# Optimization experiments

Hardware: AMD Instinct MI355X
Metric: run time of the kernel (lower is better)

Reference implementation:

```python
import jax, jax.numpy as jnp
import numpy as np

D_MODEL = 512
NUM_HEADS = 8


def setup_inputs() -> dict:
    key = jax.random.key(0)
    ks = jax.random.split(key, 6)
    B, S, D = 4, 2048, D_MODEL
    Q = jax.random.normal(ks[0], (B, S, D), dtype=jnp.float32)
    K = jax.random.normal(ks[1], (B, S, D), dtype=jnp.float32)
    V = jax.random.normal(ks[2], (B, S, D), dtype=jnp.float32)
    # boolean mask, True = masked out; random so no row is fully masked
    mask = jax.random.randint(ks[3], (B, S, S), 0, 2).astype(jnp.bool_)
    scale = 1.0 / np.sqrt(D)
    Wq = jax.random.normal(ks[4], (D, D), dtype=jnp.float32) * scale
    Wo = jax.random.normal(ks[5], (D, D), dtype=jnp.float32) * scale
    return {"Q": Q, "K": K, "V": V, "mask": mask, "Wq": Wq, "Wo": Wo}


def reference(Q, K, V, mask, Wq, Wo):
    B, S, D = Q.shape
    H = NUM_HEADS
    dk = D // H
    # Faithful to the source: Q_Linear's weight (Wq) is applied to Q, K AND V
    # (K_Linear / V_Linear are dead parameters in the original module).
    q = (Q @ Wq.T).reshape(B, S, H, dk)
    k = (K @ Wq.T).reshape(B, S, H, dk)
    v = (V @ Wq.T).reshape(B, S, H, dk)
    # scores: [B, H, Sq, Sk]
    scores = jnp.einsum("bqhd,bkhd->bhqk", q, k)
    scores = jnp.where(mask[:, None, :, :], -jnp.inf, scores)
    w = jax.nn.softmax(scores / jnp.sqrt(jnp.asarray(dk, scores.dtype)), axis=-1)
    c = jnp.einsum("bhqk,bkhd->bqhd", w, v).reshape(B, S, D)
    return c @ Wo.T
```

## Files before the change

kernel.cpp:

```cpp
#include <hip/hip_runtime.h>
#include <math.h>

#define B_ 4
#define S_ 2048
#define D_ 512
#define H_ 8
#define DK_ 64
#define MROWS (B_ * S_)

typedef short bf16x8 __attribute__((ext_vector_type(8)));
typedef float f32x4 __attribute__((ext_vector_type(4)));

static __device__ __forceinline__ unsigned short f2bf(float x) {
    unsigned int u = __float_as_uint(x);
    return (unsigned short)((u + 0x7FFFu + ((u >> 16) & 1u)) >> 16);
}
static __device__ __forceinline__ unsigned int cvt_pk_bf16(float a, float b) {
    unsigned int r;
    asm("v_cvt_pk_bf16_f32 %0, %1, %2" : "=v"(r) : "v"(a), "v"(b));
    return r;
}
static __device__ __forceinline__ float exp2_fast(float x) {
    float r;
    asm("v_exp_f32 %0, %1" : "=v"(r) : "v"(x));
    return r;
}

#define NXE (MROWS * D_)
#define NWE (D_ * D_)
#define CAST_BLOCKS ((3 * NXE + 2 * NWE) / 8 / 256)
#define MASK_BLOCKS (B_ * S_ * S_ / 256)

__global__ __launch_bounds__(256) void prep(const float* __restrict__ Q,
                                            const float* __restrict__ K,
                                            const float* __restrict__ V,
                                            const float* __restrict__ Wq,
                                            const float* __restrict__ Wo,
                                            const void* __restrict__ mask,
                                            unsigned short* __restrict__ Qb,
                                            unsigned short* __restrict__ Kb,
                                            unsigned short* __restrict__ Vb,
                                            unsigned short* __restrict__ Wqb,
                                            unsigned short* __restrict__ Wob,
                                            unsigned long long* __restrict__ mb) {
    if (blockIdx.x < CAST_BLOCKS) {
        const int NA = NXE / 8;
        const int NWn = NWE / 8;
        int id = blockIdx.x * 256 + threadIdx.x;
        const float* src;
        unsigned short* dst;
        if (id < 3 * NA) {
            int a = id / NA, r = id - a * NA;
            src = (a == 0 ? Q : a == 1 ? K : V) + (size_t)r * 8;
            dst = (a == 0 ? Qb : a == 1 ? Kb : Vb) + (size_t)r * 8;
        } else {
            int r = id - 3 * NA;
            int a = r / NWn; r -= a * NWn;
            src = (a == 0 ? Wq : Wo) + (size_t)r * 8;
            dst = (a == 0 ? Wqb : Wob) + (size_t)r * 8;
        }
        float4 x = *(const float4*)src;
        float4 y = *(const float4*)(src + 4);
        unsigned short u[8] = {f2bf(x.x), f2bf(x.y), f2bf(x.z), f2bf(x.w),
                               f2bf(y.x), f2bf(y.y), f2bf(y.z), f2bf(y.w)};
        *(uint4*)dst = *(const uint4*)u;
    } else {
        const int id = (blockIdx.x - CAST_BLOCKS) * 256 + threadIdx.x;
        unsigned int accw = 0;
        if ((threadIdx.x & 63) == 0) {
            const unsigned int* mw0 = (const unsigned int*)mask;
            #pragma unroll
            for (int i = 0; i < 16; ++i) accw |= mw0[i];
        }
        accw = __shfl(accw, 0);
        const bool bytemode = (accw & 0xFFFFFF00u) != 0u;
        int val;
        if (bytemode) val = ((const unsigned char*)mask)[id];
        else          val = ((const int*)mask)[id];
        unsigned long long w = __ballot(val != 0);
        if ((threadIdx.x & 63) == 0) mb[id >> 6] = w;
    }
}

__global__ __launch_bounds__(256) void proj3(const unsigned short* __restrict__ Qb,
                                             const unsigned short* __restrict__ Kb,
                                             const unsigned short* __restrict__ Vb,
                                             const unsigned short* __restrict__ Wqb,
                                             unsigned short* __restrict__ qs,
                                             unsigned short* __restrict__ kbo,
                                             unsigned short* __restrict__ vt) {
    __shared__ unsigned short As[128 * 40];
    __shared__ unsigned short Bs[128 * 40];
    const int t = threadIdx.x;
    const int w = t >> 6, lane = t & 63, col = lane & 15, quad = lane >> 4;
    const int bm = blockIdx.x * 128, bn = blockIdx.y * 128;
    const int z = blockIdx.z;
    const unsigned short* X = (z == 0) ? Qb : (z == 1) ? Kb : Vb;
    const int wm = (w >> 1) * 64, wn = (w & 1) * 64;
    const int srow = t >> 1, shalf = t & 1;

    const unsigned short* xg = X + (size_t)(bm + srow) * D_ + shalf * 16;
    const unsigned short* wg = Wqb + (size_t)(bn + srow) * D_ + shalf * 16;
    unsigned short* asw = &As[srow * 40 + shalf * 16];
    unsigned short* bsw = &Bs[srow * 40 + shalf * 16];

    f32x4 acc[4][4];
    #pragma unroll
    for (int i = 0; i < 4; ++i)
        #pragma unroll
        for (int j = 0; j < 4; ++j) acc[i][j] = (f32x4){0.f, 0.f, 0.f, 0.f};

    #pragma unroll 1
    for (int k0 = 0; k0 < D_; k0 += 32) {
        __syncthreads();
        {
            uint4 a0 = *(const uint4*)(xg + k0);
            uint4 a1 = *(const uint4*)(xg + k0 + 8);
            uint4 b0 = *(const uint4*)(wg + k0);
            uint4 b1 = *(const uint4*)(wg + k0 + 8);
            *(uint4*)asw = a0; *(uint4*)(asw + 8) = a1;
            *(uint4*)bsw = b0; *(uint4*)(bsw + 8) = b1;
        }
        __syncthreads();

        bf16x8 af[4], bg[4];
        #pragma unroll
        for (int i = 0; i < 4; ++i)
            af[i] = *(const bf16x8*)&As[(wm + i * 16 + col) * 40 + quad * 8];
        #pragma unroll
        for (int j = 0; j < 4; ++j)
            bg[j] = *(const bf16x8*)&Bs[(wn + j * 16 + col) * 40 + quad * 8];
        #pragma unroll
        for (int i = 0; i < 4; ++i)
            #pragma unroll
            for (int j = 0; j < 4; ++j)
                acc[i][j] = __builtin_amdgcn_mfma_f32_16x16x32_bf16(
                    af[i], bg[j], acc[i][j], 0, 0, 0);
    }

    if (z == 2) {
        #pragma unroll
        for (int i = 0; i < 4; ++i) {
            const int R = bm + wm + i * 16 + quad * 4;
            const int bb = R >> 11, s0 = R & (S_ - 1);
            #pragma unroll
            for (int j = 0; j < 4; ++j) {
                const int C = bn + wn + j * 16 + col;
                const int hh = C >> 6, dd = C & (DK_ - 1);
                ushort4 u = make_ushort4(f2bf(acc[i][j][0]), f2bf(acc[i][j][1]),
                                         f2bf(acc[i][j][2]), f2bf(acc[i][j][3]));
                *(ushort4*)&vt[(((size_t)bb * H_ + hh) * DK_ + dd) * S_ + s0] = u;
            }
        }
    } else {
        unsigned short* O = (z == 0) ? qs : kbo;
        const float scl = (z == 0) ? 0.18033688f : 1.0f;
        #pragma unroll
        for (int i = 0; i < 4; ++i)
            #pragma unroll
            for (int j = 0; j < 4; ++j) {
                const int R = bm + wm + i * 16 + quad * 4;
                const int C = bn + wn + j * 16 + col;
                #pragma unroll
                for (int r = 0; r < 4; ++r)
                    O[(size_t)(R + r) * D_ + C] = f2bf(acc[i][j][r] * scl);
            }
    }
}

__global__ __launch_bounds__(256) void gemm_out(const unsigned short* __restrict__ Xb,
                                                const unsigned short* __restrict__ Wob,
                                                float* __restrict__ Out) {
    __shared__ unsigned short As[128 * 40];
    __shared__ unsigned short Bs[128 * 40];
    const int t = threadIdx.x;
    const int w = t >> 6, lane = t & 63, col = lane & 15, quad = lane >> 4;
    const int bm = blockIdx.x * 128, bn = blockIdx.y * 128;
    const int wm = (w >> 1) * 64, wn = (w & 1) * 64;
    const int srow = t >> 1, shalf = t & 1;

    const unsigned short* xg = Xb + (size_t)(bm + srow) * D_ + shalf * 16;
    const unsigned short* wg = Wob + (size_t)(bn + srow) * D_ + shalf * 16;
    unsigned short* asw = &As[srow * 40 + shalf * 16];
    unsigned short* bsw = &Bs[srow * 40 + shalf * 16];

    f32x4 acc[4][4];
    #pragma unroll
    for (int i = 0; i < 4; ++i)
        #pragma unroll
        for (int j = 0; j < 4; ++j) acc[i][j] = (f32x4){0.f, 0.f, 0.f, 0.f};

    #pragma unroll 1
    for (int k0 = 0; k0 < D_; k0 += 32) {
        __syncthreads();
        {
            uint4 a0 = *(const uint4*)(xg + k0);
            uint4 a1 = *(const uint4*)(xg + k0 + 8);
            uint4 b0 = *(const uint4*)(wg + k0);
            uint4 b1 = *(const uint4*)(wg + k0 + 8);
            *(uint4*)asw = a0; *(uint4*)(asw + 8) = a1;
            *(uint4*)bsw = b0; *(uint4*)(bsw + 8) = b1;
        }
        __syncthreads();

        bf16x8 af[4], bg[4];
        #pragma unroll
        for (int i = 0; i < 4; ++i)
            af[i] = *(const bf16x8*)&As[(wm + i * 16 + col) * 40 + quad * 8];
        #pragma unroll
        for (int j = 0; j < 4; ++j)
            bg[j] = *(const bf16x8*)&Bs[(wn + j * 16 + col) * 40 + quad * 8];
        #pragma unroll
        for (int i = 0; i < 4; ++i)
            #pragma unroll
            for (int j = 0; j < 4; ++j)
                acc[i][j] = __builtin_amdgcn_mfma_f32_16x16x32_bf16(
                    af[i], bg[j], acc[i][j], 0, 0, 0);
    }

    #pragma unroll
    for (int i = 0; i < 4; ++i)
        #pragma unroll
        for (int j = 0; j < 4; ++j) {
            const int R = bm + wm + i * 16 + quad * 4;
            const int C = bn + wn + j * 16 + col;
            #pragma unroll
            for (int r = 0; r < 4; ++r)
                Out[(size_t)(R + r) * D_ + C] = acc[i][j][r];
        }
}

__global__ __launch_bounds__(256, 4) void attn_mfma(
        const unsigned short* __restrict__ qb,
        const unsigned short* __restrict__ kb,
        const unsigned short* __restrict__ vt,
        const unsigned long long* __restrict__ mb,
        unsigned short* __restrict__ o0,
        unsigned short* __restrict__ o1,
        float* __restrict__ l0,
        float* __restrict__ l1) {
    __shared__ unsigned short sm[18432];
    const int t = threadIdx.x;
    const int w = t >> 6;
    const int lane = t & 63;
    const int col = lane & 15;
    const int quad = lane >> 4;
    const int h = blockIdx.y;
    const int b = blockIdx.z >> 1;
    const int khalf = blockIdx.z & 1;
    const int bh = b * H_ + h;
    const int qrow0 = blockIdx.x * 128 + w * 32;

    unsigned short* opart = khalf ? o1 : o0;
    float* lpart = khalf ? l1 : l0;

    const int KS = 0;
    const int VS = 4608;
    const int PS = 9216 + w * 2304;

    const unsigned int chk = cvt_pk_bf16(1.0f, 2.0f);
    const int dlo = ((chk & 0xFFFFu) == 0x3F80u) ? 0 : 16;
    const int dhi = 16 - dlo;

    bf16x8 aQ0[2], aQ1[2];
    #pragma unroll
    for (int s = 0; s < 2; ++s) {
        const unsigned short* qp =
            qb + (size_t)(b * S_ + qrow0 + s * 16 + col) * D_ + h * DK_ + quad * 8;
        aQ0[s] = *(const bf16x8*)(qp);
        aQ1[s] = *(const bf16x8*)(qp + 32);
    }

    bf16x8 ones;
    #pragma unroll
    for (int i = 0; i < 8; ++i) ones[i] = (short)0x3F80;

    f32x4 O[2][4];
    #pragma unroll
    for (int s = 0; s < 2; ++s)
        #pragma unroll
        for (int g = 0; g < 4; ++g) O[s][g] = (f32x4){0.f, 0.f, 0.f, 0.f};
    f32x4 lacc[2];
    lacc[0] = (f32x4){0.f, 0.f, 0.f, 0.f};
    lacc[1] = (f32x4){0.f, 0.f, 0.f, 0.f};

    const int trow = t >> 2;
    const int tseg = (t & 3) * 16;
    const unsigned short* kgp = kb + (size_t)(b * S_ + trow) * D_ + h * DK_ + tseg;
    const unsigned short* vgp = vt + ((size_t)bh * DK_ + trow) * S_ + tseg;
    unsigned short* ksw = &sm[KS + trow * 72 + tseg];
    unsigned short* vsw = &sm[VS + trow * 72 + tseg];

    const float CREF = 8.656170245f;
    const int kbeg = khalf * (S_ / 2);

    #pragma unroll 1
    for (int k0 = kbeg; k0 < kbeg + S_ / 2; k0 += 64) {
        __syncthreads();
        {
            const unsigned short* g1 = kgp + (size_t)k0 * D_;
            uint4 ka0 = *(const uint4*)g1;
            uint4 ka1 = *(const uint4*)(g1 + 8);
            const unsigned short* g2 = vgp + k0;
            uint4 vb0 = *(const uint4*)g2;
            uint4 vb1 = *(const uint4*)(g2 + 8);
            *(uint4*)ksw = ka0; *(uint4*)(ksw + 8) = ka1;
            *(uint4*)vsw = vb0; *(uint4*)(vsw + 8) = vb1;
        }
        __syncthreads();

        f32x4 sc[2][4];
        #pragma unroll
        for (int g = 0; g < 4; ++g) {
            bf16x8 bk0 = *(const bf16x8*)&sm[KS + (g * 16 + col) * 72 + quad * 8];
            bf16x8 bk1 = *(const bf16x8*)&sm[KS + (g * 16 + col) * 72 + 32 + quad * 8];
            #pragma unroll
            for (int s = 0; s < 2; ++s) {
                f32x4 z = {0.f, 0.f, 0.f, 0.f};
                z = __builtin_amdgcn_mfma_f32_16x16x32_bf16(aQ0[s], bk0, z, 0, 0, 0);
                z = __builtin_amdgcn_mfma_f32_16x16x32_bf16(aQ1[s], bk1, z, 0, 0, 0);
                sc[s][g] = z;
            }
        }

        #pragma unroll
        for (int s = 0; s < 2; ++s) {
            unsigned long long mw[4];
            #pragma unroll
            for (int r = 0; r < 4; ++r)
                mw[r] = mb[(size_t)(b * S_ + qrow0 + s * 16 + quad * 4 + r) * (S_ / 64)
                           + (k0 >> 6)];
            #pragma unroll
            for (int r = 0; r < 4; ++r) {
                const unsigned long long sh = mw[r] >> col;
                const unsigned int lo = (unsigned int)sh;
                const unsigned int hi = (unsigned int)(sh >> 32);
                float p0 = exp2_fast(((lo & 1u)       ? -1e30f : sc[s][0][r]) - CREF);
                float p1 = exp2_fast(((lo & 0x10000u) ? -1e30f : sc[s][1][r]) - CREF);
                float p2 = exp2_fast(((hi & 1u)       ? -1e30f : sc[s][2][r]) - CREF);
                float p3 = exp2_fast(((hi & 0x10000u) ? -1e30f : sc[s][3][r]) - CREF);
                const unsigned int u01 = cvt_pk_bf16(p0, p1);
                const unsigned int u23 = cvt_pk_bf16(p2, p3);
                const int prow = PS + (s * 16 + quad * 4 + r) * 72 + col;
                sm[prow + dlo]      = (unsigned short)u01;
                sm[prow + dhi]      = (unsigned short)(u01 >> 16);
                sm[prow + 32 + dlo] = (unsigned short)u23;
                sm[prow + 32 + dhi] = (unsigned short)(u23 >> 16);
            }
        }
        __asm__ __volatile__("s_waitcnt lgkmcnt(0)" ::: "memory");

        bf16x8 aP0[2], aP1[2];
        #pragma unroll
        for (int s = 0; s < 2; ++s) {
            aP0[s] = *(const bf16x8*)&sm[PS + (s * 16 + col) * 72 + quad * 8];
            aP1[s] = *(const bf16x8*)&sm[PS + (s * 16 + col) * 72 + 32 + quad * 8];
        }

        #pragma unroll
        for (int s = 0; s < 2; ++s) {
            lacc[s] = __builtin_amdgcn_mfma_f32_16x16x32_bf16(aP0[s], ones, lacc[s], 0, 0, 0);
            lacc[s] = __builtin_amdgcn_mfma_f32_16x16x32_bf16(aP1[s], ones, lacc[s], 0, 0, 0);
        }

        #pragma unroll
        for (int g = 0; g < 4; ++g) {
            bf16x8 bv0 = *(const bf16x8*)&sm[VS + (g * 16 + col) * 72 + quad * 8];
            bf16x8 bv1 = *(const bf16x8*)&sm[VS + (g * 16 + col) * 72 + 32 + quad * 8];
            #pragma unroll
            for (int s = 0; s < 2; ++s) {
                O[s][g] = __builtin_amdgcn_mfma_f32_16x16x32_bf16(aP0[s], bv0, O[s][g], 0, 0, 0);
                O[s][g] = __builtin_amdgcn_mfma_f32_16x16x32_bf16(aP1[s], bv1, O[s][g], 0, 0, 0);
            }
        }
    }

    #pragma unroll
    for (int s = 0; s < 2; ++s)
        #pragma unroll
        for (int r = 0; r < 4; ++r) {
            const int row = b * S_ + qrow0 + s * 16 + quad * 4 + r;
            #pragma unroll
            for (int g = 0; g < 4; ++g)
                opart[(size_t)row * D_ + h * DK_ + g * 16 + col] = f2bf(O[s][g][r]);
            if (col == 0) lpart[(size_t)row * H_ + h] = lacc[s][r];
        }
}

__global__ __launch_bounds__(256) void combine(const unsigned short* __restrict__ o0,
                                               const unsigned short* __restrict__ o1,
                                               const float* __restrict__ l0,
                                               const float* __restrict__ l1,
                                               unsigned short* __restrict__ cb) {
    const int id = blockIdx.x * 256 + threadIdx.x;
    const size_t base = (size_t)id * 8;
    const int row = (int)(base >> 9);
    const int hh = ((int)base & (D_ - 1)) >> 6;
    uint4 ua = *(const uint4*)(o0 + base);
    uint4 ub = *(const uint4*)(o1 + base);
    const float inv = 1.0f / (l0[(size_t)row * H_ + hh] + l1[(size_t)row * H_ + hh]);
    const unsigned short* pa = (const unsigned short*)&ua;
    const unsigned short* pb = (const unsigned short*)&ub;
    unsigned short out[8];
    #pragma unroll
    for (int i = 0; i < 8; ++i) {
        float fa = __uint_as_float((unsigned int)pa[i] << 16);
        float fb = __uint_as_float((unsigned int)pb[i] << 16);
        out[i] = f2bf((fa + fb) * inv);
    }
    *(uint4*)(cb + base) = *(const uint4*)out;
}

extern "C" void kernel_launch(void* const* d_in, const int* in_sizes, int n_in,
                              void* d_out, int out_size, void* d_ws, size_t ws_size,
                              hipStream_t stream) {
    const float* Q    = (const float*)d_in[0];
    const float* K    = (const float*)d_in[1];
    const float* V    = (const float*)d_in[2];
    const void*  mask = d_in[3];
    const float* Wq   = (const float*)d_in[4];
    const float* Wo   = (const float*)d_in[5];
    float* out = (float*)d_out;

    const size_t NX = (size_t)MROWS * D_;
    const size_t NW = (size_t)D_ * D_;
    unsigned short* Qb   = (unsigned short*)d_ws;
    unsigned short* Kb   = Qb + NX;
    unsigned short* Vb   = Kb + NX;
    unsigned short* Wqb  = Vb + NX;
    unsigned short* Wob  = Wqb + NW;
    unsigned short* qbuf = Wob + NW;
    unsigned short* kbuf = qbuf + NX;
    unsigned short* vtb  = kbuf + NX;
    unsigned short* cbuf = vtb + NX;
    unsigned long long* mb = (unsigned long long*)(cbuf + NX);

    unsigned short* o0 = Qb;
    unsigned short* o1 = Kb;
    float* l0 = (float*)Vb;
    float* l1 = l0 + (size_t)MROWS * H_;

    prep<<<dim3(CAST_BLOCKS + MASK_BLOCKS), dim3(256), 0, stream>>>(
        Q, K, V, Wq, Wo, mask, Qb, Kb, Vb, Wqb, Wob, mb);

    proj3<<<dim3(MROWS / 128, D_ / 128, 3), dim3(256), 0, stream>>>(
        Qb, Kb, Vb, Wqb, qbuf, kbuf, vtb);

    attn_mfma<<<dim3(S_ / 128, H_, B_ * 2), dim3(256), 0, stream>>>(
        qbuf, kbuf, vtb, mb, o0, o1, l0, l1);

    combine<<<dim3((int)(NX / 8 / 256)), dim3(256), 0, stream>>>(o0, o1, l0, l1, cbuf);

    gemm_out<<<dim3(MROWS / 128, D_ / 128), dim3(256), 0, stream>>>(cbuf, Wob, out);
}
```

Before: 277.7 us.

## Prefetch next K/V tile into registers, remap block order, fold softmax offset into MFMA

Issues the global loads for the next K and V tile right after the current tile is stored to shared memory, so memory latency overlaps with the score and PV MFMAs instead of sitting between the barriers. The constant softmax offset is folded into the MFMA accumulator initial value, which removes a subtraction per score. Blocks are also remapped from a linear block index so that neighbouring blocks spread across batch, head and key-half combinations. The cost is more live registers for the prefetched tile under a 4-waves-per-SIMD launch bound, plus one redundant prefetch on the final iteration.

```diff
diff --git a/kernel.cpp b/kernel.cpp
--- a/kernel.cpp
+++ b/kernel.cpp
@@ -245,11 +245,15 @@
     const int lane = t & 63;
     const int col = lane & 15;
     const int quad = lane >> 4;
-    const int h = blockIdx.y;
-    const int b = blockIdx.z >> 1;
-    const int khalf = blockIdx.z & 1;
+
+    const int p = blockIdx.x + 16 * blockIdx.y + 128 * blockIdx.z;
+    const int combo = ((p & 7) << 3) | (p >> 7);
+    const int bx = (p >> 3) & 15;
+    const int khalf = combo & 1;
+    const int h = (combo >> 1) & 7;
+    const int b = combo >> 4;
     const int bh = b * H_ + h;
-    const int qrow0 = blockIdx.x * 128 + w * 32;
+    const int qrow0 = bx * 128 + w * 32;
 
     unsigned short* opart = khalf ? o1 : o0;
     float* lpart = khalf ? l1 : l0;
@@ -274,6 +278,9 @@
     bf16x8 ones;
     #pragma unroll
     for (int i = 0; i < 8; ++i) ones[i] = (short)0x3F80;
+
+    const float CREF = 8.656170245f;
+    const f32x4 zinit = (f32x4){-CREF, -CREF, -CREF, -CREF};
 
     f32x4 O[2][4];
     #pragma unroll
@@ -291,23 +298,35 @@
     unsigned short* ksw = &sm[KS + trow * 72 + tseg];
     unsigned short* vsw = &sm[VS + trow * 72 + tseg];
 
-    const float CREF = 8.656170245f;
     const int kbeg = khalf * (S_ / 2);
+    const int kend = kbeg + S_ / 2;
+
+    uint4 pk0, pk1, pv0, pv1;
+    {
+        const unsigned short* g1 = kgp + (size_t)kbeg * D_;
+        pk0 = *(const uint4*)g1;
+        pk1 = *(const uint4*)(g1 + 8);
+        const unsigned short* g2 = vgp + kbeg;
+        pv0 = *(const uint4*)g2;
+        pv1 = *(const uint4*)(g2 + 8);
+    }
 
     #pragma unroll 1
-    for (int k0 = kbeg; k0 < kbeg + S_ / 2; k0 += 64) {
-        __syncthreads();
+    for (int k0 = kbeg; k0 < kend; k0 += 64) {
+        __syncthreads();
+        *(uint4*)ksw = pk0; *(uint4*)(ksw + 8) = pk1;
+        *(uint4*)vsw = pv0; *(uint4*)(vsw + 8) = pv1;
+        __syncthreads();
+
         {
-            const unsigned short* g1 = kgp + (size_t)k0 * D_;
-            uint4 ka0 = *(const uint4*)g1;
-            uint4 ka1 = *(const uint4*)(g1 + 8);
-            const unsigned short* g2 = vgp + k0;
-            uint4 vb0 = *(const uint4*)g2;
-            uint4 vb1 = *(const uint4*)(g2 + 8);
-            *(uint4*)ksw = ka0; *(uint4*)(ksw + 8) = ka1;
-            *(uint4*)vsw = vb0; *(uint4*)(vsw + 8) = vb1;
-        }
-        __syncthreads();
+            const int kn = (k0 + 64 < kend) ? (k0 + 64) : kbeg;
+            const unsigned short* n1 = kgp + (size_t)kn * D_;
+            pk0 = *(const uint4*)n1;
+            pk1 = *(const uint4*)(n1 + 8);
+            const unsigned short* n2 = vgp + kn;
+            pv0 = *(const uint4*)n2;
+            pv1 = *(const uint4*)(n2 + 8);
+        }
 
         f32x4 sc[2][4];
         #pragma unroll
@@ -316,7 +335,7 @@
             bf16x8 bk1 = *(const bf16x8*)&sm[KS + (g * 16 + col) * 72 + 32 + quad * 8];
             #pragma unroll
             for (int s = 0; s < 2; ++s) {
-                f32x4 z = {0.f, 0.f, 0.f, 0.f};
+                f32x4 z = zinit;
                 z = __builtin_amdgcn_mfma_f32_16x16x32_bf16(aQ0[s], bk0, z, 0, 0, 0);
                 z = __builtin_amdgcn_mfma_f32_16x16x32_bf16(aQ1[s], bk1, z, 0, 0, 0);
                 sc[s][g] = z;
@@ -335,10 +354,10 @@
                 const unsigned long long sh = mw[r] >> col;
                 const unsigned int lo = (unsigned int)sh;
                 const unsigned int hi = (unsigned int)(sh >> 32);
-                float p0 = exp2_fast(((lo & 1u)       ? -1e30f : sc[s][0][r]) - CREF);
-                float p1 = exp2_fast(((lo & 0x10000u) ? -1e30f : sc[s][1][r]) - CREF);
-                float p2 = exp2_fast(((hi & 1u)       ? -1e30f : sc[s][2][r]) - CREF);
-                float p3 = exp2_fast(((hi & 0x10000u) ? -1e30f : sc[s][3][r]) - CREF);
+                float p0 = exp2_fast((lo & 1u)       ? -1e30f : sc[s][0][r]);
+                float p1 = exp2_fast((lo & 0x10000u) ? -1e30f : sc[s][1][r]);
+                float p2 = exp2_fast((hi & 1u)       ? -1e30f : sc[s][2][r]);
+                float p3 = exp2_fast((hi & 0x10000u) ? -1e30f : sc[s][3][r]);
                 const unsigned int u01 = cvt_pk_bf16(p0, p1);
                 const unsigned int u23 = cvt_pk_bf16(p2, p3);
                 const int prow = PS + (s * 16 + quad * 4 + r) * 72 + col;
```

New measurement: 279.0 us. Within noise of the previous version (+0.5%).
